# Optimization experiments

Hardware: AMD Instinct MI355X
Metric: run time of the kernel (lower is better)

The kernel has to match this reference:

```python
import jax, jax.numpy as jnp
import numpy as np

N_NODES = 100000
N_EDGES = 3200000
D_IN, D_HID, D_OUT = 128, 64, 64


def setup_inputs() -> dict:
    key = jax.random.key(0)
    ks = jax.random.split(key, 8)
    x = jax.random.normal(ks[0], (N_NODES, D_IN), dtype=jnp.float32)
    edge_index = jax.random.randint(ks[1], (2, N_EDGES), 0, N_NODES, dtype=jnp.int32)
    # Glorot-ish init for GCN weights, zero bias (PyG default)
    def w(k, fi, fo):
        s = (6.0 / (fi + fo)) ** 0.5
        return jax.random.uniform(k, (fi, fo), jnp.float32, -s, s)
    return {
        "x": x,
        "edge_index": edge_index,
        "W1": w(ks[2], D_IN, D_HID), "b1": jnp.zeros((D_HID,), jnp.float32),
        "W2": w(ks[3], D_HID, D_HID), "b2": jnp.zeros((D_HID,), jnp.float32),
        "W3": w(ks[4], D_HID, D_OUT), "b3": jnp.zeros((D_OUT,), jnp.float32),
    }


def _gcn_layer(x, W, b, src, dst, norm, num_nodes):
    # GCNConv: out[i] = sum_{j->i} norm_ji * (x W)[j] + b   (self-loops included in src/dst)
    h = x @ W                                   # [N, F_out] small GEMM
    msg = h[src] * norm[:, None]                # [E+N, F_out] gather
    out = jax.ops.segment_sum(msg, dst, num_segments=num_nodes)  # scatter-add
    return out + b


def reference(x, edge_index, W1, b1, W2, b2, W3, b3):
    n = x.shape[0]
    loop = jnp.arange(n, dtype=edge_index.dtype)
    src = jnp.concatenate([edge_index[0], loop])  # add self-loops (GCN default)
    dst = jnp.concatenate([edge_index[1], loop])
    # symmetric normalization: deg^{-1/2}[src] * deg^{-1/2}[dst]
    deg = jax.ops.segment_sum(jnp.ones_like(dst, dtype=x.dtype), dst, num_segments=n)
    dinv = jnp.where(deg > 0, jax.lax.rsqrt(deg), 0.0)
    norm = dinv[src] * dinv[dst]

    h = jax.nn.relu(_gcn_layer(x, W1, b1, src, dst, norm, n))
    h = jax.nn.relu(_gcn_layer(h, W2, b2, src, dst, norm, n))
    out = _gcn_layer(h, W3, b3, src, dst, norm, n)
    return out
```

## Files before the change

### kernel.cpp

```cpp
#include <hip/hip_runtime.h>
#include <hip/hip_bf16.h>

static inline size_t align256(size_t x) { return (x + 255) & ~(size_t)255; }

#define BSTRIDE 9216

typedef float vf2 __attribute__((ext_vector_type(2)));


__global__ void cursor_init_kernel(int* __restrict__ cursor, int nb) {
    int b = blockIdx.x * blockDim.x + threadIdx.x;
    if (b < nb) cursor[b] = b * BSTRIDE;
}

__global__ __launch_bounds__(1024) void partition_place_kernel(const int* __restrict__ src,
                                                               const int* __restrict__ dst,
                                                               int* __restrict__ cursor,
                                                               unsigned int* __restrict__ part,
                                                               int e, int nb, int tile) {
    __shared__ int hist[512];
    __shared__ int base[512];
    const int t = threadIdx.x;
    const int lo = blockIdx.x * tile;
    const int hi = min(lo + tile, e);
    for (int i = t; i < nb; i += 1024) hist[i] = 0;
    __syncthreads();
    for (int i = lo + t; i < hi; i += 1024) atomicAdd(&hist[dst[i] >> 8], 1);
    __syncthreads();
    for (int i = t; i < nb; i += 1024) {
        int c = hist[i];
        base[i] = c ? atomicAdd(&cursor[i], c) : 0;
        hist[i] = 0;
    }
    __syncthreads();
    for (int i = lo + t; i < hi; i += 1024) {
        int s = src[i], d = dst[i];
        int b = d >> 8;
        int p = base[b] + atomicAdd(&hist[b], 1);
        part[p] = ((unsigned int)s << 8) | (unsigned int)(d & 255);
    }
}

__global__ __launch_bounds__(512) void cursor_scan_kernel(const int* __restrict__ cursor,
                                                          int* __restrict__ bstart, int nb) {
    __shared__ int lds[512];
    const int t = threadIdx.x;
    int v = (t < nb) ? (cursor[t] - t * BSTRIDE) : 0;
    lds[t] = v;
    __syncthreads();
    for (int off = 1; off < 512; off <<= 1) {
        int add = (t >= off) ? lds[t - off] : 0;
        __syncthreads();
        lds[t] += add;
        __syncthreads();
    }
    if (t < nb) {
        bstart[t] = lds[t] - v;
        if (t == nb - 1) bstart[nb] = lds[t];
    }
}

__global__ __launch_bounds__(1024) void csr_build_place_kernel(const unsigned int* __restrict__ part,
                                                               const int* __restrict__ bstart,
                                                               int* __restrict__ row_ptr,
                                                               float* __restrict__ dinv,
                                                               int* __restrict__ col, int n) {
    __shared__ int cnt[256];
    __shared__ int scan[256];
    __shared__ int cur[256];
    const int t = threadIdx.x;
    const int node0 = blockIdx.x << 8;
    const int o0 = bstart[blockIdx.x];
    const int m = bstart[blockIdx.x + 1] - o0;
    const int p0 = blockIdx.x * BSTRIDE;
    if (t < 256) cnt[t] = 0;
    __syncthreads();
    for (int i = t; i < m; i += 1024) atomicAdd(&cnt[part[p0 + i] & 255u], 1);
    __syncthreads();
    const int v = (t < 256) ? cnt[t] : 0;
    if (t < 256) scan[t] = v;
    __syncthreads();
    for (int off = 1; off < 256; off <<= 1) {
        int add = (t >= off && t < 256) ? scan[t - off] : 0;
        __syncthreads();
        if (t < 256) scan[t] += add;
        __syncthreads();
    }
    if (t < 256) {
        const int node = node0 + t;
        const int excl = o0 + scan[t] - v;
        cur[t] = excl;
        if (node < n) {
            row_ptr[node] = excl;
            dinv[node] = rsqrtf((float)(v + 1));
            if (node == n - 1) row_ptr[n] = o0 + m;
        }
    }
    __syncthreads();
    for (int i = t; i < m; i += 1024) {
        unsigned int sd = part[p0 + i];
        int p = atomicAdd(&cur[sd & 255u], 1);
        col[p] = (int)(sd >> 8);
    }
}


__device__ __forceinline__ unsigned int bf16rne(float f) {
    unsigned int u = __float_as_uint(f);
    return (u + 0x7fffu + ((u >> 16) & 1u)) >> 16;
}
__device__ __forceinline__ unsigned int bf16pack(float a, float b) {
    return bf16rne(a) | (bf16rne(b) << 16);
}

__device__ __forceinline__ vf2 bf2f(unsigned int u) {
    float2 f = __bfloat1622float2(*(const __hip_bfloat162*)&u);
    vf2 r; r.x = f.x; r.y = f.y;
    return r;
}
__device__ __forceinline__ void bf8add(vf2* a, uint4 v) {
    a[0] += bf2f(v.x);
    a[1] += bf2f(v.y);
    a[2] += bf2f(v.z);
    a[3] += bf2f(v.w);
}


template<int K>
__global__ __launch_bounds__(256) void gemm_scale(const float* __restrict__ A,
                                                  const float* __restrict__ W,
                                                  const float* __restrict__ dinv,
                                                  unsigned int* __restrict__ gout, int n) {
    constexpr int KC = 64;
    constexpr int ROWS = 128;
    constexpr int LDX = KC + 4;
    __shared__ float xs[ROWS * LDX];
    __shared__ float ws[KC * 64];
    const int t = threadIdx.x;
    const int r0 = blockIdx.x * ROWS;
    const int rt = t >> 3;
    const int c4 = (t & 7) * 2;

    float acc[4][8];
#pragma unroll
    for (int a = 0; a < 4; ++a)
#pragma unroll
        for (int b = 0; b < 8; ++b) acc[a][b] = 0.f;

    for (int kc = 0; kc < K; kc += KC) {
        {
            const float4* Wg = (const float4*)(W + kc * 64);
            for (int i = t; i < KC * 16; i += 256) ((float4*)ws)[i] = Wg[i];
        }
        {
            const int jr = t >> 4;
            const int j = t & 15;
            for (int r = jr; r < ROWS; r += 16) {
                const int gr = r0 + r;
                float4 v = make_float4(0.f, 0.f, 0.f, 0.f);
                if (gr < n) v = ((const float4*)A)[(size_t)gr * (K / 4) + (kc >> 2) + j];
                *(float4*)&xs[r * LDX + j * 4] = v;
            }
        }
        __syncthreads();
#pragma unroll 4
        for (int k = 0; k < KC; ++k) {
            const float4 w0 = ((const float4*)ws)[k * 16 + c4];
            const float4 w1 = ((const float4*)ws)[k * 16 + c4 + 1];
#pragma unroll
            for (int rr = 0; rr < 4; ++rr) {
                const float xv = xs[(rt + rr * 32) * LDX + k];
                acc[rr][0] = fmaf(xv, w0.x, acc[rr][0]);
                acc[rr][1] = fmaf(xv, w0.y, acc[rr][1]);
                acc[rr][2] = fmaf(xv, w0.z, acc[rr][2]);
                acc[rr][3] = fmaf(xv, w0.w, acc[rr][3]);
                acc[rr][4] = fmaf(xv, w1.x, acc[rr][4]);
                acc[rr][5] = fmaf(xv, w1.y, acc[rr][5]);
                acc[rr][6] = fmaf(xv, w1.z, acc[rr][6]);
                acc[rr][7] = fmaf(xv, w1.w, acc[rr][7]);
            }
        }
        __syncthreads();
    }
#pragma unroll
    for (int rr = 0; rr < 4; ++rr) {
        const int gr = r0 + rt + rr * 32;
        if (gr < n) {
            const float d = dinv[gr];
            uint4 o;
            o.x = bf16pack(acc[rr][0] * d, acc[rr][1] * d);
            o.y = bf16pack(acc[rr][2] * d, acc[rr][3] * d);
            o.z = bf16pack(acc[rr][4] * d, acc[rr][5] * d);
            o.w = bf16pack(acc[rr][6] * d, acc[rr][7] * d);
            ((uint4*)gout)[(size_t)gr * 8 + (t & 7)] = o;
        }
    }
}


__device__ __forceinline__ void gather_agg8(const uint4* __restrict__ g,
                                            const int* __restrict__ row_ptr,
                                            const int* __restrict__ col,
                                            int node, int fc, vf2* acc) {
    bf8add(acc, g[(size_t)node * 8 + fc]);
    int e = row_ptr[node];
    const int e1 = row_ptr[node + 1];
    while (e < e1 && (e & 3)) { bf8add(acc, g[(size_t)col[e] * 8 + fc]); ++e; }
    int nb = (e1 - e) >> 3;
    if (nb > 0) {
        const int4* cp = (const int4*)(col + e);
        e += nb << 3;
        int4 c0 = cp[0], c1 = cp[1];
        cp += 2;
        for (int i = 1; i < nb; ++i) {
            const int4 n0 = cp[0], n1 = cp[1];
            cp += 2;
            uint4 v0 = g[(size_t)c0.x * 8 + fc];
            uint4 v1 = g[(size_t)c0.y * 8 + fc];
            uint4 v2 = g[(size_t)c0.z * 8 + fc];
            uint4 v3 = g[(size_t)c0.w * 8 + fc];
            uint4 v4 = g[(size_t)c1.x * 8 + fc];
            uint4 v5 = g[(size_t)c1.y * 8 + fc];
            uint4 v6 = g[(size_t)c1.z * 8 + fc];
            uint4 v7 = g[(size_t)c1.w * 8 + fc];
            bf8add(acc, v0); bf8add(acc, v1); bf8add(acc, v2); bf8add(acc, v3);
            bf8add(acc, v4); bf8add(acc, v5); bf8add(acc, v6); bf8add(acc, v7);
            c0 = n0; c1 = n1;
        }
        uint4 v0 = g[(size_t)c0.x * 8 + fc];
        uint4 v1 = g[(size_t)c0.y * 8 + fc];
        uint4 v2 = g[(size_t)c0.z * 8 + fc];
        uint4 v3 = g[(size_t)c0.w * 8 + fc];
        uint4 v4 = g[(size_t)c1.x * 8 + fc];
        uint4 v5 = g[(size_t)c1.y * 8 + fc];
        uint4 v6 = g[(size_t)c1.z * 8 + fc];
        uint4 v7 = g[(size_t)c1.w * 8 + fc];
        bf8add(acc, v0); bf8add(acc, v1); bf8add(acc, v2); bf8add(acc, v3);
        bf8add(acc, v4); bf8add(acc, v5); bf8add(acc, v6); bf8add(acc, v7);
    }
    if (e + 4 <= e1) {
        const int4 c0 = *(const int4*)(col + e);
        uint4 v0 = g[(size_t)c0.x * 8 + fc];
        uint4 v1 = g[(size_t)c0.y * 8 + fc];
        uint4 v2 = g[(size_t)c0.z * 8 + fc];
        uint4 v3 = g[(size_t)c0.w * 8 + fc];
        bf8add(acc, v0); bf8add(acc, v1); bf8add(acc, v2); bf8add(acc, v3);
        e += 4;
    }
    for (; e < e1; ++e) bf8add(acc, g[(size_t)col[e] * 8 + fc]);
}


__global__ __launch_bounds__(256) void fused_agg_gemm_kernel(const uint4* __restrict__ g,
                                                             const int* __restrict__ row_ptr,
                                                             const int* __restrict__ col,
                                                             const float* __restrict__ dinv,
                                                             const float* __restrict__ bias,
                                                             const float* __restrict__ W,
                                                             unsigned int* __restrict__ gout,
                                                             int n) {
    __shared__ float ws[64 * 64];
    const int t = threadIdx.x;
    const int r = t >> 3;
    const int fc = t & 7;
    const int node = blockIdx.x * 32 + r;
    const bool valid = node < n;

    for (int i = t; i < 1024; i += 256) ((float4*)ws)[i] = ((const float4*)W)[i];

    vf2 acc[4];
    acc[0] = vf2{0.f, 0.f}; acc[1] = vf2{0.f, 0.f};
    acc[2] = vf2{0.f, 0.f}; acc[3] = vf2{0.f, 0.f};
    if (valid) {
        gather_agg8(g, row_ptr, col, node, fc, acc);
        const float d = dinv[node];
        const float4 b0 = ((const float4*)bias)[fc * 2];
        const float4 b1 = ((const float4*)bias)[fc * 2 + 1];
        acc[0].x = fmaxf(fmaf(acc[0].x, d, b0.x), 0.f);
        acc[0].y = fmaxf(fmaf(acc[0].y, d, b0.y), 0.f);
        acc[1].x = fmaxf(fmaf(acc[1].x, d, b0.z), 0.f);
        acc[1].y = fmaxf(fmaf(acc[1].y, d, b0.w), 0.f);
        acc[2].x = fmaxf(fmaf(acc[2].x, d, b1.x), 0.f);
        acc[2].y = fmaxf(fmaf(acc[2].y, d, b1.y), 0.f);
        acc[3].x = fmaxf(fmaf(acc[3].x, d, b1.z), 0.f);
        acc[3].y = fmaxf(fmaf(acc[3].y, d, b1.w), 0.f);
    }
    float hr[8];
    hr[0] = acc[0].x; hr[1] = acc[0].y; hr[2] = acc[1].x; hr[3] = acc[1].y;
    hr[4] = acc[2].x; hr[5] = acc[2].y; hr[6] = acc[3].x; hr[7] = acc[3].y;

    __syncthreads();

    const int grp = (t & 63) & ~7;
    float a0 = 0.f, a1 = 0.f, a2 = 0.f, a3 = 0.f;
    float a4 = 0.f, a5 = 0.f, a6 = 0.f, a7 = 0.f;
#pragma unroll 8
    for (int k = 0; k < 64; ++k) {
        const float hv = __shfl(hr[k & 7], grp | (k >> 3), 64);
        const float4 w0 = ((const float4*)ws)[k * 16 + fc * 2];
        const float4 w1 = ((const float4*)ws)[k * 16 + fc * 2 + 1];
        a0 = fmaf(hv, w0.x, a0);
        a1 = fmaf(hv, w0.y, a1);
        a2 = fmaf(hv, w0.z, a2);
        a3 = fmaf(hv, w0.w, a3);
        a4 = fmaf(hv, w1.x, a4);
        a5 = fmaf(hv, w1.y, a5);
        a6 = fmaf(hv, w1.z, a6);
        a7 = fmaf(hv, w1.w, a7);
    }
    if (valid) {
        const float d2 = dinv[node];
        uint4 o;
        o.x = bf16pack(a0 * d2, a1 * d2);
        o.y = bf16pack(a2 * d2, a3 * d2);
        o.z = bf16pack(a4 * d2, a5 * d2);
        o.w = bf16pack(a6 * d2, a7 * d2);
        ((uint4*)gout)[(size_t)node * 8 + fc] = o;
    }
}


__global__ __launch_bounds__(256) void aggregate_kernel(const uint4* __restrict__ g,
                                                        const int* __restrict__ row_ptr,
                                                        const int* __restrict__ col,
                                                        const float* __restrict__ dinv,
                                                        const float* __restrict__ bias,
                                                        float4* __restrict__ out,
                                                        int n) {
    const int t = threadIdx.x;
    const int node = blockIdx.x * 32 + (t >> 3);
    const int fc = t & 7;
    if (node >= n) return;
    vf2 acc[4];
    acc[0] = vf2{0.f, 0.f}; acc[1] = vf2{0.f, 0.f};
    acc[2] = vf2{0.f, 0.f}; acc[3] = vf2{0.f, 0.f};
    gather_agg8(g, row_ptr, col, node, fc, acc);
    const float d = dinv[node];
    const float4 b0 = ((const float4*)bias)[fc * 2];
    const float4 b1 = ((const float4*)bias)[fc * 2 + 1];
    float4 o0, o1;
    o0.x = fmaf(acc[0].x, d, b0.x);
    o0.y = fmaf(acc[0].y, d, b0.y);
    o0.z = fmaf(acc[1].x, d, b0.z);
    o0.w = fmaf(acc[1].y, d, b0.w);
    o1.x = fmaf(acc[2].x, d, b1.x);
    o1.y = fmaf(acc[2].y, d, b1.y);
    o1.z = fmaf(acc[3].x, d, b1.z);
    o1.w = fmaf(acc[3].y, d, b1.w);
    out[(size_t)node * 16 + fc * 2]     = o0;
    out[(size_t)node * 16 + fc * 2 + 1] = o1;
}


extern "C" void kernel_launch(void* const* d_in, const int* in_sizes, int n_in,
                              void* d_out, int out_size, void* d_ws, size_t ws_size,
                              hipStream_t stream) {
    const float* x  = (const float*)d_in[0];
    const int*   ei = (const int*)d_in[1];
    const float* W1 = (const float*)d_in[2];
    const float* b1 = (const float*)d_in[3];
    const float* W2 = (const float*)d_in[4];
    const float* b2 = (const float*)d_in[5];
    const float* W3 = (const float*)d_in[6];
    const float* b3 = (const float*)d_in[7];
    float* out = (float*)d_out;

    const int n = in_sizes[0] / 128;
    const int e = in_sizes[1] / 2;
    const int* srcv = ei;
    const int* dstv = ei + e;

    char* ws = (char*)d_ws;
    size_t off = 0;
    float* dinv   = (float*)(ws + off); off = align256(off + (size_t)n * 4);
    int* row_ptr  = (int*)(ws + off);   off = align256(off + (size_t)(n + 1) * 4);
    int* bstart   = (int*)(ws + off);   off = align256(off + 1024 * 4);
    int* cursor   = (int*)(ws + off);   off = align256(off + 1024 * 4);
    int* col      = (int*)(ws + off);   off = align256(off + (size_t)e * 4);
    unsigned int* gbuf  = (unsigned int*)(ws + off); off = align256(off + (size_t)n * 64 * 2);
    unsigned int* gbuf2 = (unsigned int*)(ws + off); off = align256(off + (size_t)n * 64 * 2);
    unsigned int* part  = gbuf;
    (void)ws_size; (void)n_in; (void)out_size;

    const int nbkt = (n + 255) >> 8;

    cursor_init_kernel<<<2, 512, 0, stream>>>(cursor, nbkt);
    const int G = 400;
    const int tile = (e + G - 1) / G;
    partition_place_kernel<<<G, 1024, 0, stream>>>(srcv, dstv, cursor, part, e, nbkt, tile);
    cursor_scan_kernel<<<1, 512, 0, stream>>>(cursor, bstart, nbkt);
    csr_build_place_kernel<<<nbkt, 1024, 0, stream>>>(part, bstart, row_ptr, dinv, col, n);

    const int gemm_grid = (n + 127) / 128;
    const int agg_grid = (n + 31) / 32;

    gemm_scale<128><<<gemm_grid, 256, 0, stream>>>(x, W1, dinv, gbuf, n);
    fused_agg_gemm_kernel<<<agg_grid, 256, 0, stream>>>((const uint4*)gbuf, row_ptr, col,
                                                        dinv, b1, W2, gbuf2, n);
    fused_agg_gemm_kernel<<<agg_grid, 256, 0, stream>>>((const uint4*)gbuf2, row_ptr, col,
                                                        dinv, b2, W3, gbuf, n);
    aggregate_kernel<<<agg_grid, 256, 0, stream>>>((const uint4*)gbuf, row_ptr, col,
                                                   dinv, b3, (float4*)out, n);
}
```

Measured before the change: 405.7 us.

## Sort nodes by degree via counting sort to balance gather warps

Builds a degree histogram during CSR construction, scans it, and places nodes into a degree-sorted permutation. The aggregation kernels then process nodes in that order, so the 8 lanes per node in a wavefront see similar degrees and divergence drops. Gather addressing also switches to 32-bit byte offsets to cut address arithmetic. The cost is two extra small kernels, a global atomic per node, and scattered writes of output rows and reads of row_ptr/dinv, since adjacent threads no longer handle adjacent nodes.

```diff
diff --git a/kernel.cpp b/kernel.cpp
--- a/kernel.cpp
+++ b/kernel.cpp
@@ -8,9 +8,10 @@
 typedef float vf2 __attribute__((ext_vector_type(2)));
 
 
-__global__ void cursor_init_kernel(int* __restrict__ cursor, int nb) {
+__global__ void cursor_init_kernel(int* __restrict__ cursor, int nb, int* __restrict__ dhist) {
     int b = blockIdx.x * blockDim.x + threadIdx.x;
     if (b < nb) cursor[b] = b * BSTRIDE;
+    if (b >= 512 && b < 768) dhist[b - 512] = 0;
 }
 
 __global__ __launch_bounds__(1024) void partition_place_kernel(const int* __restrict__ src,
@@ -64,7 +65,8 @@
                                                                const int* __restrict__ bstart,
                                                                int* __restrict__ row_ptr,
                                                                float* __restrict__ dinv,
-                                                               int* __restrict__ col, int n) {
+                                                               int* __restrict__ col,
+                                                               int* __restrict__ dhist, int n) {
     __shared__ int cnt[256];
     __shared__ int scan[256];
     __shared__ int cur[256];
@@ -94,6 +96,7 @@
             row_ptr[node] = excl;
             dinv[node] = rsqrtf((float)(v + 1));
             if (node == n - 1) row_ptr[n] = o0 + m;
+            atomicAdd(&dhist[min(v, 255)], 1);
         }
     }
     __syncthreads();
@@ -101,6 +104,33 @@
         unsigned int sd = part[p0 + i];
         int p = atomicAdd(&cur[sd & 255u], 1);
         col[p] = (int)(sd >> 8);
+    }
+}
+
+__global__ __launch_bounds__(256) void dhist_scan_kernel(const int* __restrict__ dhist,
+                                                         int* __restrict__ dbase) {
+    __shared__ int lds[256];
+    const int t = threadIdx.x;
+    const int v = dhist[t];
+    lds[t] = v;
+    __syncthreads();
+    for (int off = 1; off < 256; off <<= 1) {
+        int add = (t >= off) ? lds[t - off] : 0;
+        __syncthreads();
+        lds[t] += add;
+        __syncthreads();
+    }
+    dbase[t] = lds[t] - v;
+}
+
+__global__ __launch_bounds__(256) void perm_place_kernel(const int* __restrict__ row_ptr,
+                                                         int* __restrict__ dcur,
+                                                         int* __restrict__ perm, int n) {
+    const int i = blockIdx.x * 256 + threadIdx.x;
+    if (i < n) {
+        const int deg = row_ptr[i + 1] - row_ptr[i];
+        const int p = atomicAdd(&dcur[min(deg, 255)], 1);
+        perm[p] = i;
     }
 }
 
@@ -198,14 +228,17 @@
 }
 
 
-__device__ __forceinline__ void gather_agg8(const uint4* __restrict__ g,
+__device__ __forceinline__ void gather_agg8(const char* __restrict__ gp,
                                             const int* __restrict__ row_ptr,
                                             const int* __restrict__ col,
-                                            int node, int fc, vf2* acc) {
-    bf8add(acc, g[(size_t)node * 8 + fc]);
+                                            int node, unsigned int fo, vf2* acc) {
+    bf8add(acc, *(const uint4*)(gp + ((unsigned int)node << 7) + fo));
     int e = row_ptr[node];
     const int e1 = row_ptr[node + 1];
-    while (e < e1 && (e & 3)) { bf8add(acc, g[(size_t)col[e] * 8 + fc]); ++e; }
+    while (e < e1 && (e & 3)) {
+        bf8add(acc, *(const uint4*)(gp + ((unsigned int)col[e] << 7) + fo));
+        ++e;
+    }
     int nb = (e1 - e) >> 3;
     if (nb > 0) {
         const int4* cp = (const int4*)(col + e);
@@ -215,43 +248,45 @@
         for (int i = 1; i < nb; ++i) {
             const int4 n0 = cp[0], n1 = cp[1];
             cp += 2;
-            uint4 v0 = g[(size_t)c0.x * 8 + fc];
-            uint4 v1 = g[(size_t)c0.y * 8 + fc];
-            uint4 v2 = g[(size_t)c0.z * 8 + fc];
-            uint4 v3 = g[(size_t)c0.w * 8 + fc];
-            uint4 v4 = g[(size_t)c1.x * 8 + fc];
-            uint4 v5 = g[(size_t)c1.y * 8 + fc];
-            uint4 v6 = g[(size_t)c1.z * 8 + fc];
-            uint4 v7 = g[(size_t)c1.w * 8 + fc];
+            uint4 v0 = *(const uint4*)(gp + ((unsigned int)c0.x << 7) + fo);
+            uint4 v1 = *(const uint4*)(gp + ((unsigned int)c0.y << 7) + fo);
+            uint4 v2 = *(const uint4*)(gp + ((unsigned int)c0.z << 7) + fo);
+            uint4 v3 = *(const uint4*)(gp + ((unsigned int)c0.w << 7) + fo);
+            uint4 v4 = *(const uint4*)(gp + ((unsigned int)c1.x << 7) + fo);
+            uint4 v5 = *(const uint4*)(gp + ((unsigned int)c1.y << 7) + fo);
+            uint4 v6 = *(const uint4*)(gp + ((unsigned int)c1.z << 7) + fo);
+            uint4 v7 = *(const uint4*)(gp + ((unsigned int)c1.w << 7) + fo);
             bf8add(acc, v0); bf8add(acc, v1); bf8add(acc, v2); bf8add(acc, v3);
             bf8add(acc, v4); bf8add(acc, v5); bf8add(acc, v6); bf8add(acc, v7);
             c0 = n0; c1 = n1;
         }
-        uint4 v0 = g[(size_t)c0.x * 8 + fc];
-        uint4 v1 = g[(size_t)c0.y * 8 + fc];
-        uint4 v2 = g[(size_t)c0.z * 8 + fc];
-        uint4 v3 = g[(size_t)c0.w * 8 + fc];
-        uint4 v4 = g[(size_t)c1.x * 8 + fc];
-        uint4 v5 = g[(size_t)c1.y * 8 + fc];
-        uint4 v6 = g[(size_t)c1.z * 8 + fc];
-        uint4 v7 = g[(size_t)c1.w * 8 + fc];
+        uint4 v0 = *(const uint4*)(gp + ((unsigned int)c0.x << 7) + fo);
+        uint4 v1 = *(const uint4*)(gp + ((unsigned int)c0.y << 7) + fo);
+        uint4 v2 = *(const uint4*)(gp + ((unsigned int)c0.z << 7) + fo);
+        uint4 v3 = *(const uint4*)(gp + ((unsigned int)c0.w << 7) + fo);
+        uint4 v4 = *(const uint4*)(gp + ((unsigned int)c1.x << 7) + fo);
+        uint4 v5 = *(const uint4*)(gp + ((unsigned int)c1.y << 7) + fo);
+        uint4 v6 = *(const uint4*)(gp + ((unsigned int)c1.z << 7) + fo);
+        uint4 v7 = *(const uint4*)(gp + ((unsigned int)c1.w << 7) + fo);
         bf8add(acc, v0); bf8add(acc, v1); bf8add(acc, v2); bf8add(acc, v3);
         bf8add(acc, v4); bf8add(acc, v5); bf8add(acc, v6); bf8add(acc, v7);
     }
     if (e + 4 <= e1) {
         const int4 c0 = *(const int4*)(col + e);
-        uint4 v0 = g[(size_t)c0.x * 8 + fc];
-        uint4 v1 = g[(size_t)c0.y * 8 + fc];
-        uint4 v2 = g[(size_t)c0.z * 8 + fc];
-        uint4 v3 = g[(size_t)c0.w * 8 + fc];
+        uint4 v0 = *(const uint4*)(gp + ((unsigned int)c0.x << 7) + fo);
+        uint4 v1 = *(const uint4*)(gp + ((unsigned int)c0.y << 7) + fo);
+        uint4 v2 = *(const uint4*)(gp + ((unsigned int)c0.z << 7) + fo);
+        uint4 v3 = *(const uint4*)(gp + ((unsigned int)c0.w << 7) + fo);
         bf8add(acc, v0); bf8add(acc, v1); bf8add(acc, v2); bf8add(acc, v3);
         e += 4;
     }
-    for (; e < e1; ++e) bf8add(acc, g[(size_t)col[e] * 8 + fc]);
+    for (; e < e1; ++e)
+        bf8add(acc, *(const uint4*)(gp + ((unsigned int)col[e] << 7) + fo));
 }
 
 
 __global__ __launch_bounds__(256) void fused_agg_gemm_kernel(const uint4* __restrict__ g,
+                                                             const int* __restrict__ perm,
                                                              const int* __restrict__ row_ptr,
                                                              const int* __restrict__ col,
                                                              const float* __restrict__ dinv,
@@ -263,8 +298,9 @@
     const int t = threadIdx.x;
     const int r = t >> 3;
     const int fc = t & 7;
-    const int node = blockIdx.x * 32 + r;
-    const bool valid = node < n;
+    const int gid = blockIdx.x * 32 + r;
+    const bool valid = gid < n;
+    const int node = valid ? perm[gid] : 0;
 
     for (int i = t; i < 1024; i += 256) ((float4*)ws)[i] = ((const float4*)W)[i];
 
@@ -272,7 +308,7 @@
     acc[0] = vf2{0.f, 0.f}; acc[1] = vf2{0.f, 0.f};
     acc[2] = vf2{0.f, 0.f}; acc[3] = vf2{0.f, 0.f};
     if (valid) {
-        gather_agg8(g, row_ptr, col, node, fc, acc);
+        gather_agg8((const char*)g, row_ptr, col, node, (unsigned int)fc * 16u, acc);
         const float d = dinv[node];
         const float4 b0 = ((const float4*)bias)[fc * 2];
         const float4 b1 = ((const float4*)bias)[fc * 2 + 1];
@@ -321,6 +357,7 @@
 
 
 __global__ __launch_bounds__(256) void aggregate_kernel(const uint4* __restrict__ g,
+                                                        const int* __restrict__ perm,
                                                         const int* __restrict__ row_ptr,
                                                         const int* __restrict__ col,
                                                         const float* __restrict__ dinv,
@@ -328,13 +365,14 @@
                                                         float4* __restrict__ out,
                                                         int n) {
     const int t = threadIdx.x;
-    const int node = blockIdx.x * 32 + (t >> 3);
+    const int gid = blockIdx.x * 32 + (t >> 3);
     const int fc = t & 7;
-    if (node >= n) return;
+    if (gid >= n) return;
+    const int node = perm[gid];
     vf2 acc[4];
     acc[0] = vf2{0.f, 0.f}; acc[1] = vf2{0.f, 0.f};
     acc[2] = vf2{0.f, 0.f}; acc[3] = vf2{0.f, 0.f};
-    gather_agg8(g, row_ptr, col, node, fc, acc);
+    gather_agg8((const char*)g, row_ptr, col, node, (unsigned int)fc * 16u, acc);
     const float d = dinv[node];
     const float4 b0 = ((const float4*)bias)[fc * 2];
     const float4 b1 = ((const float4*)bias)[fc * 2 + 1];
@@ -376,6 +414,9 @@
     int* row_ptr  = (int*)(ws + off);   off = align256(off + (size_t)(n + 1) * 4);
     int* bstart   = (int*)(ws + off);   off = align256(off + 1024 * 4);
     int* cursor   = (int*)(ws + off);   off = align256(off + 1024 * 4);
+    int* dhist    = (int*)(ws + off);   off = align256(off + 256 * 4);
+    int* dbase    = (int*)(ws + off);   off = align256(off + 256 * 4);
+    int* perm     = (int*)(ws + off);   off = align256(off + (size_t)n * 4);
     int* col      = (int*)(ws + off);   off = align256(off + (size_t)e * 4);
     unsigned int* gbuf  = (unsigned int*)(ws + off); off = align256(off + (size_t)n * 64 * 2);
     unsigned int* gbuf2 = (unsigned int*)(ws + off); off = align256(off + (size_t)n * 64 * 2);
@@ -384,21 +425,23 @@
 
     const int nbkt = (n + 255) >> 8;
 
-    cursor_init_kernel<<<2, 512, 0, stream>>>(cursor, nbkt);
+    cursor_init_kernel<<<2, 512, 0, stream>>>(cursor, nbkt, dhist);
     const int G = 400;
     const int tile = (e + G - 1) / G;
     partition_place_kernel<<<G, 1024, 0, stream>>>(srcv, dstv, cursor, part, e, nbkt, tile);
     cursor_scan_kernel<<<1, 512, 0, stream>>>(cursor, bstart, nbkt);
-    csr_build_place_kernel<<<nbkt, 1024, 0, stream>>>(part, bstart, row_ptr, dinv, col, n);
+    csr_build_place_kernel<<<nbkt, 1024, 0, stream>>>(part, bstart, row_ptr, dinv, col, dhist, n);
+    dhist_scan_kernel<<<1, 256, 0, stream>>>(dhist, dbase);
+    perm_place_kernel<<<(n + 255) / 256, 256, 0, stream>>>(row_ptr, dbase, perm, n);
 
     const int gemm_grid = (n + 127) / 128;
     const int agg_grid = (n + 31) / 32;
 
     gemm_scale<128><<<gemm_grid, 256, 0, stream>>>(x, W1, dinv, gbuf, n);
-    fused_agg_gemm_kernel<<<agg_grid, 256, 0, stream>>>((const uint4*)gbuf, row_ptr, col,
+    fused_agg_gemm_kernel<<<agg_grid, 256, 0, stream>>>((const uint4*)gbuf, perm, row_ptr, col,
                                                         dinv, b1, W2, gbuf2, n);
-    fused_agg_gemm_kernel<<<agg_grid, 256, 0, stream>>>((const uint4*)gbuf2, row_ptr, col,
+    fused_agg_gemm_kernel<<<agg_grid, 256, 0, stream>>>((const uint4*)gbuf2, perm, row_ptr, col,
                                                         dinv, b2, W3, gbuf, n);
-    aggregate_kernel<<<agg_grid, 256, 0, stream>>>((const uint4*)gbuf, row_ptr, col,
+    aggregate_kernel<<<agg_grid, 256, 0, stream>>>((const uint4*)gbuf, perm, row_ptr, col,
                                                    dinv, b3, (float4*)out, n);
 }
```

Result: slower. 746.2 us (+84.0%).
